# Kernel tuning notes

Measured on AMD Instinct MI355X. Metric: run time of the kernel, lower is better.

Reference implementation:

```python
import jax, jax.numpy as jnp
import numpy as np
import math

THETA = 1.0


def _qdense(xa, xb, wa, wb, ba, bb):
    # QComplexDense: j_squared = -cos(2*theta)
    j2 = -math.cos(2.0 * THETA)
    out_a = xa @ wa.T + j2 * (xb @ wb.T) + ba
    out_b = xa @ wb.T + xb @ wa.T + bb
    return out_a, out_b


def setup_inputs() -> dict:
    key = jax.random.key(0)
    B, S, D = 4, 2048, 1024
    ks = jax.random.split(key, 16)
    limit = math.sqrt(6.0 / (D + D))  # xavier uniform for square [D,D]

    def w(k):
        return jax.random.uniform(k, (D, D), jnp.float32, -limit, limit)

    inp = {
        'xa': jax.random.normal(ks[0], (B, S, D), jnp.float32),
        'xb': jax.random.normal(ks[1], (B, S, D), jnp.float32),
    }
    i = 2
    for n in ('q', 'k', 'v', 'o'):
        inp[n + '_wa'] = w(ks[i]); inp[n + '_wb'] = w(ks[i + 1])
        inp[n + '_ba'] = jnp.zeros((D,), jnp.float32)
        inp[n + '_bb'] = jnp.zeros((D,), jnp.float32)
        i += 2
    return inp


def reference(xa, xb,
              q_wa, q_wb, q_ba, q_bb,
              k_wa, k_wb, k_ba, k_bb,
              v_wa, v_wb, v_ba, v_bb,
              o_wa, o_wb, o_ba, o_bb):
    D = xa.shape[-1]
    # NOTE: qc_matmul in the original uses cos(2 * ones(1)) == cos(2.0),
    # a constant independent of theta.
    c2 = math.cos(2.0)

    Qa, Qb = _qdense(xa, xb, q_wa, q_wb, q_ba, q_bb)
    Ka, Kb = _qdense(xa, xb, k_wa, k_wb, k_ba, k_bb)
    Va, Vb = _qdense(xa, xb, v_wa, v_wb, v_ba, v_bb)

    # complex-style QK^T: scores_a = Qa Ka^T - cos(2) Qb Kb^T ; scores_b = Qa Kb^T + Qb Ka^T
    sa = jnp.einsum('bsd,btd->bst', Qa, Ka) - c2 * jnp.einsum('bsd,btd->bst', Qb, Kb)
    sb = jnp.einsum('bsd,btd->bst', Qa, Kb) + jnp.einsum('bsd,btd->bst', Qb, Ka)
    scores_real = jnp.sqrt(sa * sa + sb * sb)  # magnitude
    attn = jax.nn.softmax(scores_real / math.sqrt(D), axis=-1)  # [B,S,S]

    out_a = jnp.einsum('bst,btd->bsd', attn, Va)
    out_b = jnp.einsum('bst,btd->bsd', attn, Vb)
    return _qdense(out_a, out_b, o_wa, o_wb, o_ba, o_bb)
```

## Files before the change

### kernel.cpp

```cpp
#include <hip/hip_runtime.h>
#include <math.h>

typedef __bf16 bf16_t;
typedef __attribute__((ext_vector_type(16))) float f32x16;
typedef __attribute__((ext_vector_type(8))) __bf16 v8bf;
typedef __attribute__((ext_vector_type(4))) __bf16 v4bf;

#define GLLDS(g, l)                                                           \
  __builtin_amdgcn_global_load_lds(                                           \
      (const __attribute__((address_space(1))) void*)(g),                     \
      (__attribute__((address_space(3))) void*)(l), 16, 0, 0)
#define OPQ(p) asm volatile("" : "+v"(p))

__global__ void sentinel_kernel(float* o, float v) { o[0] = v; }

__global__ __launch_bounds__(256) void pack_x_kernel(
    const float* __restrict__ xa, const float* __restrict__ xb,
    bf16_t* __restrict__ xcat, int n4)
{
  int i = blockIdx.x * 256 + threadIdx.x;
  if (i >= n4) return;
  float4 a = reinterpret_cast<const float4*>(xa)[i];
  float4 b = reinterpret_cast<const float4*>(xb)[i];
  long e = (long)i * 4;
  long m = e >> 10;
  int  d = (int)(e & 1023);
  v4bf av = { (bf16_t)a.x, (bf16_t)a.y, (bf16_t)a.z, (bf16_t)a.w };
  v4bf bv = { (bf16_t)b.x, (bf16_t)b.y, (bf16_t)b.z, (bf16_t)b.w };
  *reinterpret_cast<v4bf*>(xcat + m * 2048 + d)        = av;
  *reinterpret_cast<v4bf*>(xcat + m * 2048 + 1024 + d) = bv;
}

__global__ __launch_bounds__(256) void pack_w_kernel(
    const float* __restrict__ wa, const float* __restrict__ wb,
    bf16_t* __restrict__ outA, bf16_t* __restrict__ outB, float j2)
{
  int i = blockIdx.x * 256 + threadIdx.x;
  float4 a = reinterpret_cast<const float4*>(wa)[i];
  float4 b = reinterpret_cast<const float4*>(wb)[i];
  long e = (long)i * 4;
  long n = e >> 10;
  int  k = (int)(e & 1023);
  v4bf av = { (bf16_t)a.x, (bf16_t)a.y, (bf16_t)a.z, (bf16_t)a.w };
  v4bf bv = { (bf16_t)b.x, (bf16_t)b.y, (bf16_t)b.z, (bf16_t)b.w };
  v4bf jb = { (bf16_t)(j2*b.x), (bf16_t)(j2*b.y), (bf16_t)(j2*b.z), (bf16_t)(j2*b.w) };
  *reinterpret_cast<v4bf*>(outA + n * 2048 + k)        = av;
  *reinterpret_cast<v4bf*>(outA + n * 2048 + 1024 + k) = jb;
  *reinterpret_cast<v4bf*>(outB + n * 2048 + k)        = bv;
  *reinterpret_cast<v4bf*>(outB + n * 2048 + 1024 + k) = av;
}

struct WPack {
  const float* wa[4];
  const float* wb[4];
  bf16_t* oA[4];
  bf16_t* oB[4];
};
__global__ __launch_bounds__(256) void pack_w4_kernel(WPack wp, float j2)
{
  const int p = blockIdx.y;
  const float* wa = wp.wa[p];
  const float* wb = wp.wb[p];
  bf16_t* outA = wp.oA[p];
  bf16_t* outB = wp.oB[p];
  int i = blockIdx.x * 256 + threadIdx.x;
  float4 a = reinterpret_cast<const float4*>(wa)[i];
  float4 b = reinterpret_cast<const float4*>(wb)[i];
  long e = (long)i * 4;
  long n = e >> 10;
  int  k = (int)(e & 1023);
  v4bf av = { (bf16_t)a.x, (bf16_t)a.y, (bf16_t)a.z, (bf16_t)a.w };
  v4bf bv = { (bf16_t)b.x, (bf16_t)b.y, (bf16_t)b.z, (bf16_t)b.w };
  v4bf jb = { (bf16_t)(j2*b.x), (bf16_t)(j2*b.y), (bf16_t)(j2*b.z), (bf16_t)(j2*b.w) };
  *reinterpret_cast<v4bf*>(outA + n * 2048 + k)        = av;
  *reinterpret_cast<v4bf*>(outA + n * 2048 + 1024 + k) = jb;
  *reinterpret_cast<v4bf*>(outB + n * 2048 + k)        = bv;
  *reinterpret_cast<v4bf*>(outB + n * 2048 + 1024 + k) = av;
}

template<int EPI>
__global__ __launch_bounds__(512) void gemm256_kernel(
    const bf16_t* __restrict__ A, const bf16_t* __restrict__ B,
    int K, long lda, long ldb, long bsA, long bsB,
    void* __restrict__ o0p, void* __restrict__ o1p, void* __restrict__ o2p,
    const float* __restrict__ bb0, const float* __restrict__ bb1,
    const float* __restrict__ bb2, const float* __restrict__ bb3,
    const float* __restrict__ bb4, const float* __restrict__ bb5,
    float scl)
{
  __shared__ __align__(16) bf16_t lds[65536];
  const int tid  = threadIdx.x;
  const int wid  = tid >> 6;
  const int lane = tid & 63;
  const int wm = wid >> 2;
  const int wn = wid & 3;

  const long row0 = (long)blockIdx.y * 256;
  const long col0 = (long)blockIdx.x * 256;
  const int z = blockIdx.z;
  const bf16_t* Ab = A + (long)z * bsA + row0 * lda;
  const bf16_t* Bb = B + (long)z * bsB + col0 * ldb;

  const int srow = wid * 8 + (lane >> 3);
  const int scol = ((lane & 7) ^ (lane >> 3)) * 8;
  const int dbase = wid * 512;

  const bf16_t* sA0 = Ab + (long)srow * lda + scol;
  const bf16_t* sA1 = Ab + (long)(srow + 64) * lda + scol;
  const bf16_t* sA2 = Ab + (long)(srow + 128) * lda + scol;
  const bf16_t* sA3 = Ab + (long)(srow + 192) * lda + scol;
  const bf16_t* sB0 = Bb + (long)srow * ldb + scol;
  const bf16_t* sB1 = Bb + (long)(srow + 64) * ldb + scol;
  const bf16_t* sB2 = Bb + (long)(srow + 128) * ldb + scol;
  const bf16_t* sB3 = Bb + (long)(srow + 192) * ldb + scol;

  const int r32 = lane & 31;
  const int kg2 = lane >> 5;
  const int r7 = r32 & 7;
  const bf16_t *pAs[4], *pBs[4];
#pragma unroll
  for (int s = 0; s < 4; ++s) {
    const int ch = (((kg2 + 2 * s) ^ r7) & 7) * 8;
    pAs[s] = lds + (wm * 128 + r32) * 64 + ch;
    pBs[s] = lds + 16384 + (wn * 64 + r32) * 64 + ch;
  }

  f32x16 acc[4][2];
#pragma unroll
  for (int i = 0; i < 4; ++i)
#pragma unroll
    for (int j = 0; j < 2; ++j)
#pragma unroll
      for (int e = 0; e < 16; ++e) acc[i][j][e] = 0.f;

  const int T = K >> 6;

  GLLDS(sA0, lds + dbase);
  GLLDS(sA1, lds + 4096 + dbase);
  GLLDS(sA2, lds + 8192 + dbase);
  GLLDS(sA3, lds + 12288 + dbase);
  GLLDS(sB0, lds + 16384 + dbase);
  GLLDS(sB1, lds + 16384 + 4096 + dbase);
  GLLDS(sB2, lds + 16384 + 8192 + dbase);
  GLLDS(sB3, lds + 16384 + 12288 + dbase);
  sA0 += 64; sA1 += 64; sA2 += 64; sA3 += 64;
  sB0 += 64; sB1 += 64; sB2 += 64; sB3 += 64;
  OPQ(sA0); OPQ(sA1); OPQ(sA2); OPQ(sA3);
  OPQ(sB0); OPQ(sB1); OPQ(sB2); OPQ(sB3);
  asm volatile("s_waitcnt vmcnt(0)" ::: "memory");
  __builtin_amdgcn_sched_barrier(0);
  __builtin_amdgcn_s_barrier();

#define TILE_BODY(U, PF)                                                       \
  {                                                                            \
    const int so_ = (U) * 32768;                                               \
    const int ns_ = (1 - (U)) * 32768;                                         \
    v8bf a_[4][2], b_[2][2];                                                   \
                                             \
    _Pragma("unroll") for (int g = 0; g < 2; ++g)                              \
      _Pragma("unroll") for (int ss = 0; ss < 2; ++ss)                         \
        b_[g][ss] = *reinterpret_cast<const v8bf*>(pBs[ss] + so_ + g * 2048);  \
    _Pragma("unroll") for (int f = 0; f < 4; ++f)                              \
      _Pragma("unroll") for (int ss = 0; ss < 2; ++ss)                         \
        a_[f][ss] = *reinterpret_cast<const v8bf*>(pAs[ss] + so_ + f * 2048);  \
    if (PF) {                                                                  \
      GLLDS(sA0, lds + ns_ + dbase);                                           \
      GLLDS(sA1, lds + ns_ + 4096 + dbase);                                    \
      GLLDS(sA2, lds + ns_ + 8192 + dbase);                                    \
      GLLDS(sA3, lds + ns_ + 12288 + dbase);                                   \
    }                                                                          \
    __builtin_amdgcn_s_setprio(1);                                             \
    _Pragma("unroll") for (int ss = 0; ss < 2; ++ss)                           \
      _Pragma("unroll") for (int f = 0; f < 4; ++f)                            \
        _Pragma("unroll") for (int g = 0; g < 2; ++g)                          \
          acc[f][g] = __builtin_amdgcn_mfma_f32_32x32x16_bf16(a_[f][ss], b_[g][ss], acc[f][g], 0, 0, 0); \
    __builtin_amdgcn_s_setprio(0);                                             \
                                             \
    _Pragma("unroll") for (int g = 0; g < 2; ++g)                              \
      _Pragma("unroll") for (int ss = 0; ss < 2; ++ss)                         \
        b_[g][ss] = *reinterpret_cast<const v8bf*>(pBs[2 + ss] + so_ + g * 2048); \
    _Pragma("unroll") for (int f = 0; f < 4; ++f)                              \
      _Pragma("unroll") for (int ss = 0; ss < 2; ++ss)                         \
        a_[f][ss] = *reinterpret_cast<const v8bf*>(pAs[2 + ss] + so_ + f * 2048); \
    if (PF) {                                                                  \
      GLLDS(sB0, lds + ns_ + 16384 + dbase);                                   \
      GLLDS(sB1, lds + ns_ + 16384 + 4096 + dbase);                            \
      GLLDS(sB2, lds + ns_ + 16384 + 8192 + dbase);                            \
      GLLDS(sB3, lds + ns_ + 16384 + 12288 + dbase);                           \
      sA0 += 64; sA1 += 64; sA2 += 64; sA3 += 64;                              \
      sB0 += 64; sB1 += 64; sB2 += 64; sB3 += 64;                              \
      OPQ(sA0); OPQ(sA1); OPQ(sA2); OPQ(sA3);                                  \
      OPQ(sB0); OPQ(sB1); OPQ(sB2); OPQ(sB3);                                  \
    }                                                                          \
    __builtin_amdgcn_s_setprio(1);                                             \
    _Pragma("unroll") for (int ss = 0; ss < 2; ++ss)                           \
      _Pragma("unroll") for (int f = 0; f < 4; ++f)                            \
        _Pragma("unroll") for (int g = 0; g < 2; ++g)                          \
          acc[f][g] = __builtin_amdgcn_mfma_f32_32x32x16_bf16(a_[f][ss], b_[g][ss], acc[f][g], 0, 0, 0); \
    __builtin_amdgcn_s_setprio(0);                                             \
    asm volatile("s_waitcnt vmcnt(0)" ::: "memory");                           \
    __builtin_amdgcn_sched_barrier(0);                                         \
    __builtin_amdgcn_s_barrier();                                              \
  }

  for (int tb = 0; tb < T - 2; tb += 2) {
    TILE_BODY(0, 1)
    TILE_BODY(1, 1)
  }
  TILE_BODY(0, 1)
  TILE_BODY(1, 0)
#undef TILE_BODY

  const int hi = lane >> 5;
#pragma unroll
  for (int fm = 0; fm < 4; ++fm) {
#pragma unroll
    for (int fn = 0; fn < 2; ++fn) {
      const f32x16 v = acc[fm][fn];
      const long rowb = row0 + wm * 128 + fm * 32 + 4 * hi;
      const long col  = col0 + wn * 64 + fn * 32 + r32;
      if constexpr (EPI == 0) {
        const int  seg = (int)(col >> 10);
        const long c   = col & 1023;
        bf16_t* Q  = (bf16_t*)o0p;
        bf16_t* Kc = (bf16_t*)o1p;
        bf16_t* Vc = (bf16_t*)o2p;
        switch (seg) {
          case 0: { const float bv = bb0[c];
#pragma unroll
            for (int r = 0; r < 16; ++r) {
              const long row = rowb + (r & 3) + 8 * (r >> 2);
              Q[row * 2048 + c] = (bf16_t)((v[r] + bv) * 0.03125f);
            } } break;
          case 1: { const float bv = bb1[c];
#pragma unroll
            for (int r = 0; r < 16; ++r) {
              const long row = rowb + (r & 3) + 8 * (r >> 2);
              Q[row * 2048 + 1024 + c] = (bf16_t)((v[r] + bv) * 0.03125f);
            } } break;
          case 2: { const float bv = bb2[c];
#pragma unroll
            for (int r = 0; r < 16; ++r) {
              const long row = rowb + (r & 3) + 8 * (r >> 2);
              const long kb2 = (row >> 11) * 8388608 + (row & 2047) * 4096;
              const float w = v[r] + bv;
              Kc[kb2 + c]               = (bf16_t)w;
              Kc[kb2 + 2048 + 1024 + c] = (bf16_t)w;
            } } break;
          case 3: { const float bv = bb3[c];
#pragma unroll
            for (int r = 0; r < 16; ++r) {
              const long row = rowb + (r & 3) + 8 * (r >> 2);
              const long kb2 = (row >> 11) * 8388608 + (row & 2047) * 4096;
              const float w = v[r] + bv;
              Kc[kb2 + 2048 + c] = (bf16_t)w;
              Kc[kb2 + 1024 + c] = (bf16_t)(scl * w);
            } } break;
          case 4: { const float bv = bb4[c];
#pragma unroll
            for (int r = 0; r < 16; ++r) {
              const long row = rowb + (r & 3) + 8 * (r >> 2);
              Vc[row * 2048 + c] = (bf16_t)(v[r] + bv);
            } } break;
          default: { const float bv = bb5[c];
#pragma unroll
            for (int r = 0; r < 16; ++r) {
              const long row = rowb + (r & 3) + 8 * (r >> 2);
              Vc[row * 2048 + 1024 + c] = (bf16_t)(v[r] + bv);
            } } break;
        }
      } else if constexpr (EPI == 1) {
        bf16_t* dst = (bf16_t*)o0p;
        const long tt = col >> 1;
        float mg[16];
#pragma unroll
        for (int r = 0; r < 16; ++r) {
          const float x = v[r];
          const float p = __shfl_xor(x, 1);
          mg[r] = sqrtf(x * x + p * p);
        }
        const int rb2 = (lane & 1) * 8;
#pragma unroll
        for (int rr2 = 0; rr2 < 8; ++rr2) {
          const int r = rb2 + rr2;
          const long row = rowb + (r & 3) + 8 * (r >> 2);
          dst[(long)z * 4194304 + row * 2048 + tt] = (bf16_t)mg[r];
        }
      } else if constexpr (EPI == 2) {
#pragma unroll
        for (int r = 0; r < 16; ++r) {
          const long row = rowb + (r & 3) + 8 * (r >> 2);
          ((bf16_t*)o0p)[(long)z * 4194304 + row * 2048 + col] = (bf16_t)v[r];
        }
      } else {
        const int  seg = (int)(col >> 10);
        const long c   = col & 1023;
        float* dst = seg ? (float*)o1p : (float*)o0p;
        const float bv = seg ? bb1[c] : bb0[c];
#pragma unroll
        for (int r = 0; r < 16; ++r) {
          const long row = rowb + (r & 3) + 8 * (r >> 2);
          dst[row * 1024 + c] = v[r] + bv;
        }
      }
    }
  }
}

__global__ __launch_bounds__(256) void transpose_v_kernel(
    const bf16_t* __restrict__ src, bf16_t* __restrict__ dst)
{
  __shared__ bf16_t t[64][65];
  const int tid = threadIdx.x;
  const int off = blockIdx.z * 1024;
  const long c0 = (long)blockIdx.x * 64;
  const long g0 = (long)blockIdx.y * 64;
#pragma unroll
  for (int it = 0; it < 16; ++it) {
    int idx = it * 256 + tid;
    int r = idx >> 6, c = idx & 63;
    t[r][c] = src[(g0 + r) * 2048 + off + c0 + c];
  }
  __syncthreads();
  const long b  = g0 >> 11;
  const long t0 = g0 & 2047;
#pragma unroll
  for (int it = 0; it < 16; ++it) {
    int idx = it * 256 + tid;
    int nr = idx >> 6, tc = idx & 63;
    dst[b * 4194304 + (off + c0 + nr) * 2048 + t0 + tc] = t[tc][nr];
  }
}

__global__ __launch_bounds__(256) void softmax_kernel(
    const bf16_t* __restrict__ mag, bf16_t* __restrict__ attn)
{
  const int tid = threadIdx.x;
  const long base = (long)blockIdx.x * 2048;
  v4bf m0 = *reinterpret_cast<const v4bf*>(mag + base + tid * 4);
  v4bf m1 = *reinterpret_cast<const v4bf*>(mag + base + 1024 + tid * 4);
  float r[8];
#pragma unroll
  for (int k = 0; k < 4; ++k) r[k] = (float)m0[k];
#pragma unroll
  for (int k = 0; k < 4; ++k) r[4 + k] = (float)m1[k];
  float m = r[0];
#pragma unroll
  for (int k = 1; k < 8; ++k) m = fmaxf(m, r[k]);
#pragma unroll
  for (int off = 32; off > 0; off >>= 1) m = fmaxf(m, __shfl_xor(m, off));
  __shared__ float red[8];
  if ((tid & 63) == 0) red[tid >> 6] = m;
  __syncthreads();
  m = fmaxf(fmaxf(red[0], red[1]), fmaxf(red[2], red[3]));
  float p[8], s = 0.f;
#pragma unroll
  for (int k = 0; k < 8; ++k) { p[k] = __expf(r[k] - m); s += p[k]; }
#pragma unroll
  for (int off = 32; off > 0; off >>= 1) s += __shfl_xor(s, off);
  if ((tid & 63) == 0) red[4 + (tid >> 6)] = s;
  __syncthreads();
  const float inv = 1.f / (red[4] + red[5] + red[6] + red[7]);
  v4bf o0 = { (bf16_t)(p[0]*inv), (bf16_t)(p[1]*inv), (bf16_t)(p[2]*inv), (bf16_t)(p[3]*inv) };
  v4bf o1 = { (bf16_t)(p[4]*inv), (bf16_t)(p[5]*inv), (bf16_t)(p[6]*inv), (bf16_t)(p[7]*inv) };
  *reinterpret_cast<v4bf*>(attn + base + tid * 4)        = o0;
  *reinterpret_cast<v4bf*>(attn + base + 1024 + tid * 4) = o1;
}

extern "C" void kernel_launch(void* const* d_in, const int* in_sizes, int n_in,
                              void* d_out, int out_size, void* d_ws, size_t ws_size,
                              hipStream_t stream)
{
  (void)in_sizes; (void)n_in; (void)out_size;
  const float* xa = (const float*)d_in[0];
  const float* xb = (const float*)d_in[1];
  const float *w_a[4], *w_b[4], *b_a[4], *b_b[4];
  for (int p = 0; p < 4; ++p) {
    w_a[p] = (const float*)d_in[2 + p*4 + 0];
    w_b[p] = (const float*)d_in[2 + p*4 + 1];
    b_a[p] = (const float*)d_in[2 + p*4 + 2];
    b_b[p] = (const float*)d_in[2 + p*4 + 3];
  }
  float* out = (float*)d_out;
  const float neg_c2 = (float)(-cos(2.0));

  const size_t WFULL = 33554432ull;
  const size_t WQKV  = 25165824ull;
  int NB = 0; bool fullW = true;
  if      (ws_size >= WFULL + 6ull * 4ull * 8388608ull) NB = 4;
  else if (ws_size >= WFULL + 6ull * 2ull * 8388608ull) NB = 2;
  else if (ws_size >= WFULL + 6ull * 1ull * 8388608ull) NB = 1;
  else if (ws_size >= WQKV  + 6ull * 1ull * 8388608ull) { NB = 1; fullW = false; }
  else { sentinel_kernel<<<1, 1, 0, stream>>>(out, (float)ws_size); return; }

  char* ws = (char*)d_ws;
  const size_t wbytes = fullW ? WFULL : WQKV;
  const size_t RB = (size_t)NB * 8388608ull;
  bf16_t* Wqkv = (bf16_t*)ws;
  bf16_t* Wo   = fullW ? (bf16_t*)(ws + WQKV) : Wqkv;
  bf16_t* R0 = (bf16_t*)(ws + wbytes);
  bf16_t* R1 = (bf16_t*)(ws + wbytes + 1*RB);
  bf16_t* Kc = (bf16_t*)(ws + wbytes + 2*RB);
  bf16_t* R4 = (bf16_t*)(ws + wbytes + 4*RB);
  bf16_t* R5 = (bf16_t*)(ws + wbytes + 5*RB);

  const int  Mc = NB * 2048;
  const dim3 blk(256);
  const dim3 blk512(512);
  const dim3 gqkv(24, Mc / 256, 1);
  const dim3 gsc(16, 8, NB);
  const dim3 gpv(8, 8, NB);
  const dim3 go(8, Mc / 256, 1);
  const dim3 gtr(16, Mc / 64, 2);

  if (fullW) {
    WPack wp;
    for (int p = 0; p < 3; ++p) {
      wp.wa[p] = w_a[p];
      wp.wb[p] = w_b[p];
      wp.oA[p] = Wqkv + (size_t)(2*p)   * 2097152ull;
      wp.oB[p] = Wqkv + (size_t)(2*p+1) * 2097152ull;
    }
    wp.wa[3] = w_a[3]; wp.wb[3] = w_b[3];
    wp.oA[3] = Wo; wp.oB[3] = Wo + 2097152ull;
    pack_w4_kernel<<<dim3(1024, 4), blk, 0, stream>>>(wp, neg_c2);
  }

  for (int c = 0; c < 4 / NB; ++c) {
    const size_t xoff = (size_t)c * NB * 2097152ull;
    pack_x_kernel<<<Mc, blk, 0, stream>>>(xa + xoff, xb + xoff, R0, Mc * 256);

    if (!fullW)
      for (int p = 0; p < 3; ++p)
        pack_w_kernel<<<1024, blk, 0, stream>>>(w_a[p], w_b[p],
            Wqkv + (size_t)(2*p)   * 2097152ull,
            Wqkv + (size_t)(2*p+1) * 2097152ull, neg_c2);

    gemm256_kernel<0><<<gqkv, blk512, 0, stream>>>(R0, Wqkv, 2048, 2048, 2048, 0, 0,
        R1, Kc, R4, b_a[0], b_b[0], b_a[1], b_b[1], b_a[2], b_b[2], neg_c2);

    transpose_v_kernel<<<gtr, blk, 0, stream>>>(R4, R5);

    gemm256_kernel<1><<<gsc, blk512, 0, stream>>>(R1, Kc, 2048, 2048, 2048, 4194304, 8388608,
        R0, nullptr, nullptr, nullptr, nullptr, nullptr, nullptr, nullptr, nullptr, 0.f);

    softmax_kernel<<<Mc, blk, 0, stream>>>(R0, R0);

    gemm256_kernel<2><<<gpv, blk512, 0, stream>>>(R0, R5, 2048, 2048, 2048, 4194304, 4194304,
        R1, nullptr, nullptr, nullptr, nullptr, nullptr, nullptr, nullptr, nullptr, 0.f);

    if (!fullW)
      pack_w_kernel<<<1024, blk, 0, stream>>>(w_a[3], w_b[3], Wo, Wo + 2097152ull, neg_c2);
    gemm256_kernel<3><<<go, blk512, 0, stream>>>(R1, Wo, 2048, 2048, 2048, 0, 0,
        out + xoff, out + 8388608ull + xoff, nullptr,
        b_a[3], b_b[3], nullptr, nullptr, nullptr, nullptr, 0.f);
  }
}
```

Baseline: 565.9 us.

## Shrink GEMM tiles to 256x128x32 with 4-wave blocks for two blocks per CU

New measurement: 615.0 us. 8.7% more time.

```diff
diff --git a/kernel.cpp b/kernel.cpp
--- a/kernel.cpp
+++ b/kernel.cpp
@@ -79,7 +79,7 @@
 }
 
 template<int EPI>
-__global__ __launch_bounds__(512) void gemm256_kernel(
+__global__ __launch_bounds__(256, 2) void gemm256_kernel(
     const bf16_t* __restrict__ A, const bf16_t* __restrict__ B,
     int K, long lda, long ldb, long bsA, long bsB,
     void* __restrict__ o0p, void* __restrict__ o1p, void* __restrict__ o2p,
@@ -88,21 +88,21 @@
     const float* __restrict__ bb4, const float* __restrict__ bb5,
     float scl)
 {
-  __shared__ __align__(16) bf16_t lds[65536];
+  __shared__ __align__(16) bf16_t lds[24576];
   const int tid  = threadIdx.x;
   const int wid  = tid >> 6;
   const int lane = tid & 63;
-  const int wm = wid >> 2;
-  const int wn = wid & 3;
+  const int wm = wid >> 1;
+  const int wn = wid & 1;
 
   const long row0 = (long)blockIdx.y * 256;
-  const long col0 = (long)blockIdx.x * 256;
+  const long col0 = (long)blockIdx.x * 128;
   const int z = blockIdx.z;
   const bf16_t* Ab = A + (long)z * bsA + row0 * lda;
   const bf16_t* Bb = B + (long)z * bsB + col0 * ldb;
 
-  const int srow = wid * 8 + (lane >> 3);
-  const int scol = ((lane & 7) ^ (lane >> 3)) * 8;
+  const int srow = tid >> 2;
+  const int scol = ((tid & 3) ^ ((tid >> 3) & 3)) * 8;
   const int dbase = wid * 512;
 
   const bf16_t* sA0 = Ab + (long)srow * lda + scol;
@@ -111,18 +111,16 @@
   const bf16_t* sA3 = Ab + (long)(srow + 192) * lda + scol;
   const bf16_t* sB0 = Bb + (long)srow * ldb + scol;
   const bf16_t* sB1 = Bb + (long)(srow + 64) * ldb + scol;
-  const bf16_t* sB2 = Bb + (long)(srow + 128) * ldb + scol;
-  const bf16_t* sB3 = Bb + (long)(srow + 192) * ldb + scol;
 
   const int r32 = lane & 31;
   const int kg2 = lane >> 5;
-  const int r7 = r32 & 7;
-  const bf16_t *pAs[4], *pBs[4];
-#pragma unroll
-  for (int s = 0; s < 4; ++s) {
-    const int ch = (((kg2 + 2 * s) ^ r7) & 7) * 8;
-    pAs[s] = lds + (wm * 128 + r32) * 64 + ch;
-    pBs[s] = lds + 16384 + (wn * 64 + r32) * 64 + ch;
+  const int key = (r32 >> 1) & 3;
+  const bf16_t *pA[2], *pB[2];
+#pragma unroll
+  for (int s = 0; s < 2; ++s) {
+    const int ch = ((s * 2 + kg2) ^ key) * 8;
+    pA[s] = lds + (wm * 128 + r32) * 32 + ch;
+    pB[s] = lds + 8192 + (wn * 64 + r32) * 32 + ch;
   }
 
   f32x16 acc[4][2];
@@ -133,70 +131,52 @@
 #pragma unroll
       for (int e = 0; e < 16; ++e) acc[i][j][e] = 0.f;
 
-  const int T = K >> 6;
+  const int T = K >> 5;
 
   GLLDS(sA0, lds + dbase);
-  GLLDS(sA1, lds + 4096 + dbase);
-  GLLDS(sA2, lds + 8192 + dbase);
-  GLLDS(sA3, lds + 12288 + dbase);
-  GLLDS(sB0, lds + 16384 + dbase);
-  GLLDS(sB1, lds + 16384 + 4096 + dbase);
-  GLLDS(sB2, lds + 16384 + 8192 + dbase);
-  GLLDS(sB3, lds + 16384 + 12288 + dbase);
-  sA0 += 64; sA1 += 64; sA2 += 64; sA3 += 64;
-  sB0 += 64; sB1 += 64; sB2 += 64; sB3 += 64;
-  OPQ(sA0); OPQ(sA1); OPQ(sA2); OPQ(sA3);
-  OPQ(sB0); OPQ(sB1); OPQ(sB2); OPQ(sB3);
+  GLLDS(sA1, lds + 2048 + dbase);
+  GLLDS(sA2, lds + 4096 + dbase);
+  GLLDS(sA3, lds + 6144 + dbase);
+  GLLDS(sB0, lds + 8192 + dbase);
+  GLLDS(sB1, lds + 10240 + dbase);
+  sA0 += 32; sA1 += 32; sA2 += 32; sA3 += 32; sB0 += 32; sB1 += 32;
+  OPQ(sA0); OPQ(sA1); OPQ(sA2); OPQ(sA3); OPQ(sB0); OPQ(sB1);
   asm volatile("s_waitcnt vmcnt(0)" ::: "memory");
   __builtin_amdgcn_sched_barrier(0);
   __builtin_amdgcn_s_barrier();
 
 #define TILE_BODY(U, PF)                                                       \
   {                                                                            \
-    const int so_ = (U) * 32768;                                               \
-    const int ns_ = (1 - (U)) * 32768;                                         \
+    const int so_ = (U) * 12288;                                               \
+    const int ns_ = (1 - (U)) * 12288;                                         \
     v8bf a_[4][2], b_[2][2];                                                   \
-                                             \
     _Pragma("unroll") for (int g = 0; g < 2; ++g)                              \
       _Pragma("unroll") for (int ss = 0; ss < 2; ++ss)                         \
-        b_[g][ss] = *reinterpret_cast<const v8bf*>(pBs[ss] + so_ + g * 2048);  \
+        b_[g][ss] = *reinterpret_cast<const v8bf*>(pB[ss] + so_ + g * 1024);   \
     _Pragma("unroll") for (int f = 0; f < 4; ++f)                              \
       _Pragma("unroll") for (int ss = 0; ss < 2; ++ss)                         \
-        a_[f][ss] = *reinterpret_cast<const v8bf*>(pAs[ss] + so_ + f * 2048);  \
+        a_[f][ss] = *reinterpret_cast<const v8bf*>(pA[ss] + so_ + f * 1024);   \
     if (PF) {                                                                  \
       GLLDS(sA0, lds + ns_ + dbase);                                           \
-      GLLDS(sA1, lds + ns_ + 4096 + dbase);                                    \
-      GLLDS(sA2, lds + ns_ + 8192 + dbase);                                    \
-      GLLDS(sA3, lds + ns_ + 12288 + dbase);                                   \
+      GLLDS(sA1, lds + ns_ + 2048 + dbase);                                    \
+      GLLDS(sA2, lds + ns_ + 4096 + dbase);                                    \
+      GLLDS(sA3, lds + ns_ + 6144 + dbase);                                    \
     }                                                                          \
     __builtin_amdgcn_s_setprio(1);                                             \
-    _Pragma("unroll") for (int ss = 0; ss < 2; ++ss)                           \
-      _Pragma("unroll") for (int f = 0; f < 4; ++f)                            \
-        _Pragma("unroll") for (int g = 0; g < 2; ++g)                          \
-          acc[f][g] = __builtin_amdgcn_mfma_f32_32x32x16_bf16(a_[f][ss], b_[g][ss], acc[f][g], 0, 0, 0); \
+    _Pragma("unroll") for (int f = 0; f < 4; ++f)                              \
+      _Pragma("unroll") for (int g = 0; g < 2; ++g)                            \
+        acc[f][g] = __builtin_amdgcn_mfma_f32_32x32x16_bf16(a_[f][0], b_[g][0], acc[f][g], 0, 0, 0); \
     __builtin_amdgcn_s_setprio(0);                                             \
-                                             \
-    _Pragma("unroll") for (int g = 0; g < 2; ++g)                              \
-      _Pragma("unroll") for (int ss = 0; ss < 2; ++ss)                         \
-        b_[g][ss] = *reinterpret_cast<const v8bf*>(pBs[2 + ss] + so_ + g * 2048); \
-    _Pragma("unroll") for (int f = 0; f < 4; ++f)                              \
-      _Pragma("unroll") for (int ss = 0; ss < 2; ++ss)                         \
-        a_[f][ss] = *reinterpret_cast<const v8bf*>(pAs[2 + ss] + so_ + f * 2048); \
     if (PF) {                                                                  \
-      GLLDS(sB0, lds + ns_ + 16384 + dbase);                                   \
-      GLLDS(sB1, lds + ns_ + 16384 + 4096 + dbase);                            \
-      GLLDS(sB2, lds + ns_ + 16384 + 8192 + dbase);                            \
-      GLLDS(sB3, lds + ns_ + 16384 + 12288 + dbase);                           \
-      sA0 += 64; sA1 += 64; sA2 += 64; sA3 += 64;                              \
-      sB0 += 64; sB1 += 64; sB2 += 64; sB3 += 64;                              \
-      OPQ(sA0); OPQ(sA1); OPQ(sA2); OPQ(sA3);                                  \
-      OPQ(sB0); OPQ(sB1); OPQ(sB2); OPQ(sB3);                                  \
+      GLLDS(sB0, lds + ns_ + 8192 + dbase);                                    \
+      GLLDS(sB1, lds + ns_ + 10240 + dbase);                                   \
+      sA0 += 32; sA1 += 32; sA2 += 32; sA3 += 32; sB0 += 32; sB1 += 32;        \
+      OPQ(sA0); OPQ(sA1); OPQ(sA2); OPQ(sA3); OPQ(sB0); OPQ(sB1);              \
     }                                                                          \
     __builtin_amdgcn_s_setprio(1);                                             \
-    _Pragma("unroll") for (int ss = 0; ss < 2; ++ss)                           \
-      _Pragma("unroll") for (int f = 0; f < 4; ++f)                            \
-        _Pragma("unroll") for (int g = 0; g < 2; ++g)                          \
-          acc[f][g] = __builtin_amdgcn_mfma_f32_32x32x16_bf16(a_[f][ss], b_[g][ss], acc[f][g], 0, 0, 0); \
+    _Pragma("unroll") for (int f = 0; f < 4; ++f)                              \
+      _Pragma("unroll") for (int g = 0; g < 2; ++g)                            \
+        acc[f][g] = __builtin_amdgcn_mfma_f32_32x32x16_bf16(a_[f][1], b_[g][1], acc[f][g], 0, 0, 0); \
     __builtin_amdgcn_s_setprio(0);                                             \
     asm volatile("s_waitcnt vmcnt(0)" ::: "memory");                           \
     __builtin_amdgcn_sched_barrier(0);                                         \
@@ -406,11 +386,10 @@
 
   const int  Mc = NB * 2048;
   const dim3 blk(256);
-  const dim3 blk512(512);
-  const dim3 gqkv(24, Mc / 256, 1);
-  const dim3 gsc(16, 8, NB);
-  const dim3 gpv(8, 8, NB);
-  const dim3 go(8, Mc / 256, 1);
+  const dim3 gqkv(48, Mc / 256, 1);
+  const dim3 gsc(32, 8, NB);
+  const dim3 gpv(16, 8, NB);
+  const dim3 go(16, Mc / 256, 1);
   const dim3 gtr(16, Mc / 64, 2);
 
   if (fullW) {
@@ -436,22 +415,22 @@
             Wqkv + (size_t)(2*p)   * 2097152ull,
             Wqkv + (size_t)(2*p+1) * 2097152ull, neg_c2);
 
-    gemm256_kernel<0><<<gqkv, blk512, 0, stream>>>(R0, Wqkv, 2048, 2048, 2048, 0, 0,
+    gemm256_kernel<0><<<gqkv, blk, 0, stream>>>(R0, Wqkv, 2048, 2048, 2048, 0, 0,
         R1, Kc, R4, b_a[0], b_b[0], b_a[1], b_b[1], b_a[2], b_b[2], neg_c2);
 
     transpose_v_kernel<<<gtr, blk, 0, stream>>>(R4, R5);
 
-    gemm256_kernel<1><<<gsc, blk512, 0, stream>>>(R1, Kc, 2048, 2048, 2048, 4194304, 8388608,
+    gemm256_kernel<1><<<gsc, blk, 0, stream>>>(R1, Kc, 2048, 2048, 2048, 4194304, 8388608,
         R0, nullptr, nullptr, nullptr, nullptr, nullptr, nullptr, nullptr, nullptr, 0.f);
 
     softmax_kernel<<<Mc, blk, 0, stream>>>(R0, R0);
 
-    gemm256_kernel<2><<<gpv, blk512, 0, stream>>>(R0, R5, 2048, 2048, 2048, 4194304, 4194304,
+    gemm256_kernel<2><<<gpv, blk, 0, stream>>>(R0, R5, 2048, 2048, 2048, 4194304, 4194304,
         R1, nullptr, nullptr, nullptr, nullptr, nullptr, nullptr, nullptr, nullptr, 0.f);
 
     if (!fullW)
       pack_w_kernel<<<1024, blk, 0, stream>>>(w_a[3], w_b[3], Wo, Wo + 2097152ull, neg_c2);
-    gemm256_kernel<3><<<go, blk512, 0, stream>>>(R1, Wo, 2048, 2048, 2048, 0, 0,
+    gemm256_kernel<3><<<go, blk, 0, stream>>>(R1, Wo, 2048, 2048, 2048, 0, 0,
         out + xoff, out + 8388608ull + xoff, nullptr,
         b_a[3], b_b[3], nullptr, nullptr, nullptr, nullptr, 0.f);
   }
```
